# Kernel optimization log

Measured on AMD Instinct MI355X. Metric: run time of the kernel, lower is better.

The kernel has to match this reference:

```python
import jax, jax.numpy as jnp
import numpy as np
from jax.ops import segment_sum

N = 100000   # total nodes
M = 50000    # propagated subset size (len(index))
E = 600000   # edges over the subset graph
D = 128      # embedding_size
EPS = 1e-8
N_LAYERS = 3  # self.LayerNums


def setup_inputs() -> dict:
    key = jax.random.key(0)
    ks = jax.random.split(key, 12)
    features = jax.random.normal(ks[0], (N, D), dtype=jnp.float32)
    index = jnp.arange(M, dtype=jnp.int64)  # subset of nodes that get propagated
    edge_row = jax.random.randint(ks[1], (E,), 0, M, dtype=jnp.int64)
    edge_col = jax.random.randint(ks[2], (E,), 0, M, dtype=jnp.int64)
    edge_val = jax.random.uniform(ks[3], (E,), dtype=jnp.float32)
    # MLP prediction weights: D -> D//2 -> D//4 -> D//6 -> 1 (last no bias)
    def xavier(k, fan_in, fan_out):
        lim = jnp.sqrt(6.0 / (fan_in + fan_out)).astype(jnp.float32)
        return jax.random.uniform(k, (fan_in, fan_out), jnp.float32, -lim, lim)
    W1 = xavier(ks[4], D, D // 2); b1 = jnp.zeros((D // 2,), jnp.float32)
    W2 = xavier(ks[5], D // 2, D // 4); b2 = jnp.zeros((D // 4,), jnp.float32)
    W3 = xavier(ks[6], D // 4, D // 6); b3 = jnp.zeros((D // 6,), jnp.float32)
    W4 = xavier(ks[7], D // 6, 1)
    return {"features": features, "index": index, "edge_row": edge_row,
            "edge_col": edge_col, "edge_val": edge_val,
            "W1": W1, "b1": b1, "W2": W2, "b2": b2, "W3": W3, "b3": b3, "W4": W4}


def _gcn_layer(features, index, row, col, val):
    # symmetric normalization: d = rowsum(A)+eps; A' = d^-1/2 A d^-1/2
    deg = segment_sum(val, row, num_segments=M)
    d_inv_sqrt = jax.lax.rsqrt(deg + EPS)
    nval = val * d_inv_sqrt[row] * d_inv_sqrt[col]
    sub = features[index]                      # [M, D] subset_features
    msg = sub[col] * nval[:, None]             # [E, D]
    out = segment_sum(msg, row, num_segments=M)  # spmm -> [M, D]
    # new_features[index] = out; untouched rows keep original features
    return features.at[index].set(out)


def reference(features, index, edge_row, edge_col, edge_val,
              W1, b1, W2, b2, W3, b3, W4):
    x = features
    for _ in range(N_LAYERS):
        x = _gcn_layer(x, index, edge_row, edge_col, edge_val)
    # MLP prediction head (eval mode: dropout off), LeakyReLU slope 0.01
    h = jax.nn.leaky_relu(x @ W1 + b1, 0.01)
    h = jax.nn.leaky_relu(h @ W2 + b2, 0.01)
    h = jax.nn.leaky_relu(h @ W3 + b3, 0.01)
    return jax.nn.sigmoid(h @ W4)              # [N, 1]
```

## Files before the change

kernel.cpp:

```cpp
#include <hip/hip_runtime.h>
#include <math.h>

#define NN 100000
#define MM 50000
#define EE 600000
#define DD 128
#define NB 196

typedef short bf16x8 __attribute__((ext_vector_type(8)));
typedef float f32x4 __attribute__((ext_vector_type(4)));

__device__ __forceinline__ float bl(unsigned u) { return __uint_as_float(u << 16); }
__device__ __forceinline__ float bh(unsigned u) { return __uint_as_float(u & 0xFFFF0000u); }
__device__ __forceinline__ unsigned rne(float f) {
    unsigned u = __float_as_uint(f);
    return (u + 0x7FFFu + ((u >> 16) & 1u)) >> 16;
}
__device__ __forceinline__ unsigned pk2(float a, float b) { return rne(a) | (rne(b) << 16); }

__device__ __forceinline__ void fmab8(float v, uint4 u, float* a) {
    a[0] = fmaf(v, bl(u.x), a[0]); a[1] = fmaf(v, bh(u.x), a[1]);
    a[2] = fmaf(v, bl(u.y), a[2]); a[3] = fmaf(v, bh(u.y), a[3]);
    a[4] = fmaf(v, bl(u.z), a[4]); a[5] = fmaf(v, bh(u.z), a[5]);
    a[6] = fmaf(v, bl(u.w), a[6]); a[7] = fmaf(v, bh(u.w), a[7]);
}

__device__ __forceinline__ void fma21(float h, const float* wrow, float* a) {
    #pragma unroll
    for (int j = 0; j < 21; ++j) a[j] = fmaf(h, wrow[j], a[j]);
}

__global__ void deg_count_kernel(const int* __restrict__ row, const float* __restrict__ val,
                                 unsigned long long* __restrict__ dcpack,
                                 int* __restrict__ slot, int* __restrict__ invidx) {
    int e = blockIdx.x * 256 + threadIdx.x;
    if (e < NN) invidx[e] = -1;
    if (e < EE) {
        int r = row[e];
        unsigned long long add = (1ULL << 44) | (unsigned long long)(val[e] * 4294967296.0f);
        unsigned long long old = atomicAdd(&dcpack[r], add);
        slot[e] = (int)(old >> 44);
    }
}

__global__ void fused_setup_kernel(const unsigned long long* __restrict__ dcpack,
                                   float* __restrict__ dis,
                                   const int* __restrict__ index, int* __restrict__ invidx,
                                   int* __restrict__ cnt, int* __restrict__ partial,
                                   int* __restrict__ bsum) {
    __shared__ int ws[4];
    int tid = threadIdx.x, lane = tid & 63, w = tid >> 6;
    int i = blockIdx.x * 256 + tid;
    int v = 0;
    if (i < MM) {
        unsigned long long pkv = dcpack[i];
        v = (int)(pkv >> 44);
        float dsum = (float)(pkv & ((1ULL << 44) - 1)) * (1.0f / 4294967296.0f);
        dis[i] = rsqrtf(dsum + 1e-8f);
        invidx[index[i]] = i;
        cnt[i] = v;
    }
    int x = v;
    #pragma unroll
    for (int off = 1; off < 64; off <<= 1) {
        int t = __shfl_up(x, off, 64);
        if (lane >= off) x += t;
    }
    if (lane == 63) ws[w] = x;
    __syncthreads();
    int add = 0;
    for (int q = 0; q < w; ++q) add += ws[q];
    x += add;
    if (i < MM) partial[i] = x;
    if (tid == 255) bsum[blockIdx.x] = x;
}

__global__ void scanB_kernel(const int* __restrict__ bsum, int* __restrict__ boff) {
    int lane = threadIdx.x;
    int carry = 0;
    for (int base = 0; base < NB; base += 64) {
        int v = (base + lane < NB) ? bsum[base + lane] : 0;
        int x = v;
        #pragma unroll
        for (int off = 1; off < 64; off <<= 1) {
            int t = __shfl_up(x, off, 64);
            if (lane >= off) x += t;
        }
        if (base + lane < NB) boff[base + lane] = carry + x - v;
        carry += __shfl(x, 63);
    }
}

__global__ void scanC_kernel(const int* __restrict__ partial, const int* __restrict__ cnt,
                             const int* __restrict__ boff, int* __restrict__ rowptr) {
    int i = blockIdx.x * 256 + threadIdx.x;
    if (i < MM) rowptr[i] = partial[i] - cnt[i] + boff[i >> 8];
    if (i == 0) rowptr[MM] = EE;
}

__global__ void scatter_kernel(const int* __restrict__ row, const int* __restrict__ col,
                               const float* __restrict__ val, const float* __restrict__ dis,
                               const int* __restrict__ rowptr, const int* __restrict__ slot,
                               int* __restrict__ col_s, float* __restrict__ val_s) {
    int e = blockIdx.x * 256 + threadIdx.x;
    if (e < EE) {
        int r = row[e], c = col[e];
        int pos = rowptr[r] + slot[e];
        col_s[pos] = c;
        val_s[pos] = val[e] * dis[r] * dis[c];
    }
}

__global__ void cvt_kernel(const float* __restrict__ feat, const int* __restrict__ index,
                           unsigned* __restrict__ X0b,
                           const float* __restrict__ W1, const float* __restrict__ W2,
                           unsigned* __restrict__ W1b, unsigned* __restrict__ W2b) {
    int i = blockIdx.x * 256 + threadIdx.x;
    if (i < MM * 64) {
        int node = i >> 6, k2 = i & 63;
        int idx = index[node];
        float2 f = ((const float2*)feat)[(size_t)idx * 64 + k2];
        X0b[i] = pk2(f.x, f.y);
    }
    if (i < 4096) {
        int j = i >> 6, kp = i & 63;
        W1b[i] = pk2(W1[(2 * kp) * 64 + j], W1[(2 * kp + 1) * 64 + j]);
    } else if (i < 5120) {
        int u = i - 4096;
        int j = u >> 5, kp = u & 31;
        W2b[u] = pk2(W2[(2 * kp) * 32 + j], W2[(2 * kp + 1) * 32 + j]);
    }
}

__global__ __launch_bounds__(256) void spmm_kernel(
    const int* __restrict__ rowptr, const int* __restrict__ cols,
    const float* __restrict__ vals, const unsigned short* __restrict__ X,
    unsigned short* __restrict__ Y) {
    int lane = threadIdx.x & 63;
    int wid = threadIdx.x >> 6;
    int g = lane >> 4, sub = lane & 15;
    int r = blockIdx.x * 16 + wid * 4 + g;
    bool valid = (r < MM);
    int rc = valid ? r : (MM - 1);
    int s = rowptr[rc], e = rowptr[rc + 1];
    const uint4* __restrict__ X4 = (const uint4*)X;
    float a[8] = {0.f, 0.f, 0.f, 0.f, 0.f, 0.f, 0.f, 0.f};
    for (int base = s; base < e; base += 16) {
        int cnt = min(16, e - base);
        int c = 0; float v = 0.f;
        if (sub < cnt) { c = cols[base + sub]; v = vals[base + sub]; }
        int j = 0;
        for (; j + 4 <= cnt; j += 4) {
            int c0 = __shfl(c, g * 16 + j);     float v0 = __shfl(v, g * 16 + j);
            int c1 = __shfl(c, g * 16 + j + 1); float v1 = __shfl(v, g * 16 + j + 1);
            int c2 = __shfl(c, g * 16 + j + 2); float v2 = __shfl(v, g * 16 + j + 2);
            int c3 = __shfl(c, g * 16 + j + 3); float v3 = __shfl(v, g * 16 + j + 3);
            uint4 u0 = X4[(size_t)c0 * 16 + sub];
            uint4 u1 = X4[(size_t)c1 * 16 + sub];
            uint4 u2 = X4[(size_t)c2 * 16 + sub];
            uint4 u3 = X4[(size_t)c3 * 16 + sub];
            fmab8(v0, u0, a);
            fmab8(v1, u1, a);
            fmab8(v2, u2, a);
            fmab8(v3, u3, a);
        }
        for (; j < cnt; ++j) {
            int cc = __shfl(c, g * 16 + j); float vv = __shfl(v, g * 16 + j);
            uint4 u0 = X4[(size_t)cc * 16 + sub];
            fmab8(vv, u0, a);
        }
    }
    if (valid) {
        uint4 o;
        o.x = pk2(a[0], a[1]); o.y = pk2(a[2], a[3]);
        o.z = pk2(a[4], a[5]); o.w = pk2(a[6], a[7]);
        ((uint4*)Y)[(size_t)r * 16 + sub] = o;
    }
}

#define NPB 64
#define XDW 68
#define WDW 36

__global__ __launch_bounds__(256) void mlp_kernel(
    const float* __restrict__ feat, const unsigned short* __restrict__ X3,
    const int* __restrict__ invidx,
    const unsigned* __restrict__ W1b, const float* __restrict__ b1,
    const unsigned* __restrict__ W2b, const float* __restrict__ b2,
    const float* __restrict__ W3, const float* __restrict__ b3,
    const float* __restrict__ W4, float* __restrict__ out) {
    __shared__ unsigned smem[4352 + 4352 + 1152];
    unsigned* xs  = smem;
    float*    h1f = (float*)smem;
    unsigned* w1t = smem + 4352;
    float*    h2f = (float*)(smem + 4352);
    unsigned* w2t = smem + 4352 + 4352;

    int tid = threadIdx.x;
    int nb = blockIdx.x * NPB;

    #pragma unroll 4
    for (int it = 0; it < 16; ++it) {
        int i = it * 256 + tid;
        int node = i >> 6, u = i & 63;
        int n = nb + node;
        unsigned p = 0;
        if (n < NN) {
            int q = invidx[n];
            if (q >= 0) p = ((const unsigned*)X3)[(size_t)q * 64 + u];
            else { float2 f = ((const float2*)feat)[(size_t)n * 64 + u]; p = pk2(f.x, f.y); }
        }
        xs[node * XDW + u] = p;
    }
    #pragma unroll
    for (int it = 0; it < 4; ++it) {
        int i = it * 256 + tid;
        int j = i >> 4, s4 = i & 15;
        uint4 wv = ((const uint4*)W1b)[i];
        *(uint4*)(w1t + j * XDW + s4 * 4) = wv;
    }
    {
        int j = tid >> 3, s4 = tid & 7;
        uint4 wv = ((const uint4*)W2b)[tid];
        *(uint4*)(w2t + j * WDW + s4 * 4) = wv;
    }
    __syncthreads();

    int lane = tid & 63, w = tid >> 6;
    int p = lane & 15, q = lane >> 4;

    bf16x8 af[4];
    #pragma unroll
    for (int kc = 0; kc < 4; ++kc)
        af[kc] = *(const bf16x8*)((const short*)(xs + (w * 16 + p) * XDW + kc * 16 + q * 4));

    f32x4 acc[4];
    #pragma unroll
    for (int jt = 0; jt < 4; ++jt) {
        float bv = b1[jt * 16 + p];
        acc[jt][0] = bv; acc[jt][1] = bv; acc[jt][2] = bv; acc[jt][3] = bv;
    }
    #pragma unroll
    for (int jt = 0; jt < 4; ++jt) {
        #pragma unroll
        for (int kc = 0; kc < 4; ++kc) {
            bf16x8 bf = *(const bf16x8*)((const short*)(w1t + (jt * 16 + p) * XDW + kc * 16 + q * 4));
            acc[jt] = __builtin_amdgcn_mfma_f32_16x16x32_bf16(af[kc], bf, acc[jt], 0, 0, 0);
        }
    }
    __syncthreads();
    #pragma unroll
    for (int jt = 0; jt < 4; ++jt) {
        #pragma unroll
        for (int r = 0; r < 4; ++r) {
            float v = acc[jt][r];
            v = v > 0.f ? v : 0.01f * v;
            h1f[(w * 16 + q * 4 + r) * XDW + jt * 16 + p] = v;
        }
    }
    __syncthreads();

    bf16x8 a2f[2];
    #pragma unroll
    for (int kc = 0; kc < 2; ++kc) {
        const float* hp = h1f + (w * 16 + p) * XDW + kc * 32 + q * 8;
        f32x4 v0 = *(const f32x4*)hp;
        f32x4 v1 = *(const f32x4*)(hp + 4);
        unsigned u0 = pk2(v0[0], v0[1]), u1 = pk2(v0[2], v0[3]);
        unsigned u2 = pk2(v1[0], v1[1]), u3 = pk2(v1[2], v1[3]);
        uint4 uu = make_uint4(u0, u1, u2, u3);
        a2f[kc] = *(const bf16x8*)&uu;
    }
    f32x4 acc2[2];
    #pragma unroll
    for (int jt = 0; jt < 2; ++jt) {
        float bv = b2[jt * 16 + p];
        acc2[jt][0] = bv; acc2[jt][1] = bv; acc2[jt][2] = bv; acc2[jt][3] = bv;
        #pragma unroll
        for (int kc = 0; kc < 2; ++kc) {
            bf16x8 bf = *(const bf16x8*)((const short*)(w2t + (jt * 16 + p) * WDW + kc * 16 + q * 4));
            acc2[jt] = __builtin_amdgcn_mfma_f32_16x16x32_bf16(a2f[kc], bf, acc2[jt], 0, 0, 0);
        }
    }
    __syncthreads();
    #pragma unroll
    for (int jt = 0; jt < 2; ++jt) {
        #pragma unroll
        for (int r = 0; r < 4; ++r) {
            float v = acc2[jt][r];
            v = v > 0.f ? v : 0.01f * v;
            h2f[(w * 16 + q * 4 + r) * WDW + jt * 16 + p] = v;
        }
    }
    __syncthreads();

    int node = w * 16 + p;
    float a3[21];
    #pragma unroll
    for (int j = 0; j < 21; ++j) a3[j] = b3[j];
    #pragma unroll 4
    for (int k = 0; k < 32; ++k) {
        float hk = h2f[node * WDW + k];
        fma21(hk, W3 + k * 21, a3);
    }
    float s = 0.f;
    #pragma unroll
    for (int j = 0; j < 21; ++j) {
        float vj = a3[j] > 0.f ? a3[j] : 0.01f * a3[j];
        s = fmaf(vj, W4[j], s);
    }
    if (q == 0) {
        int n = nb + node;
        if (n < NN) out[n] = 1.f / (1.f + expf(-s));
    }
}

extern "C" void kernel_launch(void* const* d_in, const int* in_sizes, int n_in,
                              void* d_out, int out_size, void* d_ws, size_t ws_size,
                              hipStream_t stream) {
    const float* feat = (const float*)d_in[0];
    const int*   index = (const int*)d_in[1];
    const int*   erow = (const int*)d_in[2];
    const int*   ecol = (const int*)d_in[3];
    const float* evalp = (const float*)d_in[4];
    const float* W1 = (const float*)d_in[5];
    const float* b1 = (const float*)d_in[6];
    const float* W2 = (const float*)d_in[7];
    const float* b2 = (const float*)d_in[8];
    const float* W3 = (const float*)d_in[9];
    const float* b3 = (const float*)d_in[10];
    const float* W4 = (const float*)d_in[11];
    float* out = (float*)d_out;

    char* ws = (char*)d_ws;
    size_t off = 0;
    auto alloc = [&](size_t bytes) -> void* {
        void* p = ws + off;
        off += (bytes + 255) & ~(size_t)255;
        return p;
    };
    unsigned long long* dcpack = (unsigned long long*)alloc((size_t)MM * 8);
    float* dis     = (float*)alloc((size_t)MM * 4);
    int*   cnt     = (int*)  alloc((size_t)MM * 4);
    int*   rowptr  = (int*)  alloc((size_t)(MM + 1) * 4);
    int*   partial = (int*)  alloc((size_t)MM * 4);
    int*   bsum    = (int*)  alloc((size_t)NB * 4);
    int*   boff    = (int*)  alloc((size_t)NB * 4);
    int*   slot    = (int*)  alloc((size_t)EE * 4);
    int*   col_s   = (int*)  alloc((size_t)EE * 4);
    float* val_s   = (float*)alloc((size_t)EE * 4);
    int*   invidx  = (int*)  alloc((size_t)NN * 4);
    unsigned* W1b  = (unsigned*)alloc(4096 * 4);
    unsigned* W2b  = (unsigned*)alloc(1024 * 4);
    unsigned*       X0b = (unsigned*)      alloc((size_t)MM * DD * 2);
    unsigned short* Xa  = (unsigned short*)alloc((size_t)MM * DD * 2);
    unsigned short* Xb  = (unsigned short*)alloc((size_t)MM * DD * 2);

    hipMemsetAsync(dcpack, 0, (size_t)MM * 8, stream);

    deg_count_kernel<<<(EE + 255) / 256, 256, 0, stream>>>(erow, evalp, dcpack, slot, invidx);
    fused_setup_kernel<<<NB, 256, 0, stream>>>(dcpack, dis, index, invidx, cnt, partial, bsum);
    scanB_kernel<<<1, 64, 0, stream>>>(bsum, boff);
    scanC_kernel<<<(MM + 255) / 256, 256, 0, stream>>>(partial, cnt, boff, rowptr);
    scatter_kernel<<<(EE + 255) / 256, 256, 0, stream>>>(erow, ecol, evalp, dis,
                                                         rowptr, slot, col_s, val_s);
    cvt_kernel<<<(MM * 64 + 255) / 256, 256, 0, stream>>>(feat, index, X0b, W1, W2, W1b, W2b);

    spmm_kernel<<<(MM + 15) / 16, 256, 0, stream>>>(rowptr, col_s, val_s,
                                                    (const unsigned short*)X0b, Xa);
    spmm_kernel<<<(MM + 15) / 16, 256, 0, stream>>>(rowptr, col_s, val_s, Xa, Xb);
    spmm_kernel<<<(MM + 15) / 16, 256, 0, stream>>>(rowptr, col_s, val_s, Xb, Xa);

    mlp_kernel<<<(NN + NPB - 1) / NPB, 256, 0, stream>>>(feat, Xa, invidx,
                                                         W1b, b1, W2b, b2, W3, b3, W4, out);
}
```

Baseline: 269.9 us.

## Write final layer into full bf16 feature buffer and simplify MLP loads

The cvt kernel now also converts the untouched (non-indexed) feature rows to bf16 in a full-size buffer, and the last SpMM writes its rows through the index remap into that same buffer. The MLP kernel then reads a single contiguous bf16 matrix straight from global memory into MFMA operands, with no shared-memory staging of X and weights and no block-wide barriers, using per-wave scratch only. This removes the per-element invidx branch and the fp32 conversion from the MLP, at the cost of a larger cvt kernel over all N rows and an extra full-size workspace buffer.

After: 265.5 us. About the same (-1.6%).

```diff
diff --git a/kernel.cpp b/kernel.cpp
--- a/kernel.cpp
+++ b/kernel.cpp
@@ -6,6 +6,7 @@
 #define EE 600000
 #define DD 128
 #define NB 196
+#define NNP 100096
 
 typedef short bf16x8 __attribute__((ext_vector_type(8)));
 typedef float f32x4 __attribute__((ext_vector_type(4)));
@@ -112,30 +113,35 @@
 }
 
 __global__ void cvt_kernel(const float* __restrict__ feat, const int* __restrict__ index,
-                           unsigned* __restrict__ X0b,
+                           const int* __restrict__ invidx,
+                           unsigned* __restrict__ X0b, unsigned* __restrict__ Xfull,
                            const float* __restrict__ W1, const float* __restrict__ W2,
                            unsigned* __restrict__ W1b, unsigned* __restrict__ W2b) {
     int i = blockIdx.x * 256 + threadIdx.x;
+    int n = i >> 6, u = i & 63;
+    if (n < NN && invidx[n] < 0) {
+        float2 f = ((const float2*)feat)[(size_t)n * 64 + u];
+        Xfull[(size_t)n * 64 + u] = pk2(f.x, f.y);
+    }
     if (i < MM * 64) {
-        int node = i >> 6, k2 = i & 63;
-        int idx = index[node];
-        float2 f = ((const float2*)feat)[(size_t)idx * 64 + k2];
+        int idx = index[n];
+        float2 f = ((const float2*)feat)[(size_t)idx * 64 + u];
         X0b[i] = pk2(f.x, f.y);
     }
     if (i < 4096) {
         int j = i >> 6, kp = i & 63;
         W1b[i] = pk2(W1[(2 * kp) * 64 + j], W1[(2 * kp + 1) * 64 + j]);
     } else if (i < 5120) {
-        int u = i - 4096;
-        int j = u >> 5, kp = u & 31;
-        W2b[u] = pk2(W2[(2 * kp) * 32 + j], W2[(2 * kp + 1) * 32 + j]);
+        int t = i - 4096;
+        int j = t >> 5, kp = t & 31;
+        W2b[t] = pk2(W2[(2 * kp) * 32 + j], W2[(2 * kp + 1) * 32 + j]);
     }
 }
 
 __global__ __launch_bounds__(256) void spmm_kernel(
     const int* __restrict__ rowptr, const int* __restrict__ cols,
     const float* __restrict__ vals, const unsigned short* __restrict__ X,
-    unsigned short* __restrict__ Y) {
+    unsigned short* __restrict__ Y, const int* __restrict__ remap) {
     int lane = threadIdx.x & 63;
     int wid = threadIdx.x >> 6;
     int g = lane >> 4, sub = lane & 15;
@@ -171,69 +177,34 @@
         }
     }
     if (valid) {
+        int dst = remap ? remap[rc] : rc;
         uint4 o;
         o.x = pk2(a[0], a[1]); o.y = pk2(a[2], a[3]);
         o.z = pk2(a[4], a[5]); o.w = pk2(a[6], a[7]);
-        ((uint4*)Y)[(size_t)r * 16 + sub] = o;
-    }
-}
-
-#define NPB 64
-#define XDW 68
-#define WDW 36
+        ((uint4*)Y)[(size_t)dst * 16 + sub] = o;
+    }
+}
 
 __global__ __launch_bounds__(256) void mlp_kernel(
-    const float* __restrict__ feat, const unsigned short* __restrict__ X3,
-    const int* __restrict__ invidx,
+    const unsigned* __restrict__ Xfull,
     const unsigned* __restrict__ W1b, const float* __restrict__ b1,
     const unsigned* __restrict__ W2b, const float* __restrict__ b2,
     const float* __restrict__ W3, const float* __restrict__ b3,
     const float* __restrict__ W4, float* __restrict__ out) {
-    __shared__ unsigned smem[4352 + 4352 + 1152];
-    unsigned* xs  = smem;
-    float*    h1f = (float*)smem;
-    unsigned* w1t = smem + 4352;
-    float*    h2f = (float*)(smem + 4352);
-    unsigned* w2t = smem + 4352 + 4352;
-
+    __shared__ float hls[4 * 1088];
     int tid = threadIdx.x;
-    int nb = blockIdx.x * NPB;
-
-    #pragma unroll 4
-    for (int it = 0; it < 16; ++it) {
-        int i = it * 256 + tid;
-        int node = i >> 6, u = i & 63;
-        int n = nb + node;
-        unsigned p = 0;
-        if (n < NN) {
-            int q = invidx[n];
-            if (q >= 0) p = ((const unsigned*)X3)[(size_t)q * 64 + u];
-            else { float2 f = ((const float2*)feat)[(size_t)n * 64 + u]; p = pk2(f.x, f.y); }
-        }
-        xs[node * XDW + u] = p;
-    }
-    #pragma unroll
-    for (int it = 0; it < 4; ++it) {
-        int i = it * 256 + tid;
-        int j = i >> 4, s4 = i & 15;
-        uint4 wv = ((const uint4*)W1b)[i];
-        *(uint4*)(w1t + j * XDW + s4 * 4) = wv;
-    }
-    {
-        int j = tid >> 3, s4 = tid & 7;
-        uint4 wv = ((const uint4*)W2b)[tid];
-        *(uint4*)(w2t + j * WDW + s4 * 4) = wv;
-    }
-    __syncthreads();
-
     int lane = tid & 63, w = tid >> 6;
     int p = lane & 15, q = lane >> 4;
+    float* hw = hls + w * 1088;
+    int nb = blockIdx.x * 64;
+    int node = nb + w * 16 + p;
 
     bf16x8 af[4];
     #pragma unroll
-    for (int kc = 0; kc < 4; ++kc)
-        af[kc] = *(const bf16x8*)((const short*)(xs + (w * 16 + p) * XDW + kc * 16 + q * 4));
-
+    for (int kc = 0; kc < 4; ++kc) {
+        uint4 u = *(const uint4*)(Xfull + (size_t)node * 64 + kc * 16 + q * 4);
+        af[kc] = *(const bf16x8*)&u;
+    }
     f32x4 acc[4];
     #pragma unroll
     for (int jt = 0; jt < 4; ++jt) {
@@ -244,31 +215,28 @@
     for (int jt = 0; jt < 4; ++jt) {
         #pragma unroll
         for (int kc = 0; kc < 4; ++kc) {
-            bf16x8 bf = *(const bf16x8*)((const short*)(w1t + (jt * 16 + p) * XDW + kc * 16 + q * 4));
+            uint4 u = *(const uint4*)(W1b + (jt * 16 + p) * 64 + kc * 16 + q * 4);
+            bf16x8 bf = *(const bf16x8*)&u;
             acc[jt] = __builtin_amdgcn_mfma_f32_16x16x32_bf16(af[kc], bf, acc[jt], 0, 0, 0);
         }
     }
-    __syncthreads();
     #pragma unroll
     for (int jt = 0; jt < 4; ++jt) {
         #pragma unroll
         for (int r = 0; r < 4; ++r) {
             float v = acc[jt][r];
             v = v > 0.f ? v : 0.01f * v;
-            h1f[(w * 16 + q * 4 + r) * XDW + jt * 16 + p] = v;
-        }
-    }
-    __syncthreads();
-
+            hw[(q * 4 + r) * 68 + jt * 16 + p] = v;
+        }
+    }
     bf16x8 a2f[2];
     #pragma unroll
     for (int kc = 0; kc < 2; ++kc) {
-        const float* hp = h1f + (w * 16 + p) * XDW + kc * 32 + q * 8;
+        const float* hp = hw + p * 68 + kc * 32 + q * 8;
         f32x4 v0 = *(const f32x4*)hp;
         f32x4 v1 = *(const f32x4*)(hp + 4);
-        unsigned u0 = pk2(v0[0], v0[1]), u1 = pk2(v0[2], v0[3]);
-        unsigned u2 = pk2(v1[0], v1[1]), u3 = pk2(v1[2], v1[3]);
-        uint4 uu = make_uint4(u0, u1, u2, u3);
+        uint4 uu = make_uint4(pk2(v0[0], v0[1]), pk2(v0[2], v0[3]),
+                              pk2(v1[0], v1[1]), pk2(v1[2], v1[3]));
         a2f[kc] = *(const bf16x8*)&uu;
     }
     f32x4 acc2[2];
@@ -278,29 +246,26 @@
         acc2[jt][0] = bv; acc2[jt][1] = bv; acc2[jt][2] = bv; acc2[jt][3] = bv;
         #pragma unroll
         for (int kc = 0; kc < 2; ++kc) {
-            bf16x8 bf = *(const bf16x8*)((const short*)(w2t + (jt * 16 + p) * WDW + kc * 16 + q * 4));
+            uint4 u = *(const uint4*)(W2b + (jt * 16 + p) * 32 + kc * 16 + q * 4);
+            bf16x8 bf = *(const bf16x8*)&u;
             acc2[jt] = __builtin_amdgcn_mfma_f32_16x16x32_bf16(a2f[kc], bf, acc2[jt], 0, 0, 0);
         }
     }
-    __syncthreads();
     #pragma unroll
     for (int jt = 0; jt < 2; ++jt) {
         #pragma unroll
         for (int r = 0; r < 4; ++r) {
             float v = acc2[jt][r];
             v = v > 0.f ? v : 0.01f * v;
-            h2f[(w * 16 + q * 4 + r) * WDW + jt * 16 + p] = v;
-        }
-    }
-    __syncthreads();
-
-    int node = w * 16 + p;
+            hw[(q * 4 + r) * 36 + jt * 16 + p] = v;
+        }
+    }
     float a3[21];
     #pragma unroll
     for (int j = 0; j < 21; ++j) a3[j] = b3[j];
     #pragma unroll 4
     for (int k = 0; k < 32; ++k) {
-        float hk = h2f[node * WDW + k];
+        float hk = hw[p * 36 + k];
         fma21(hk, W3 + k * 21, a3);
     }
     float s = 0.f;
@@ -310,7 +275,7 @@
         s = fmaf(vj, W4[j], s);
     }
     if (q == 0) {
-        int n = nb + node;
+        int n = nb + w * 16 + p;
         if (n < NN) out[n] = 1.f / (1.f + expf(-s));
     }
 }
@@ -352,9 +317,10 @@
     int*   invidx  = (int*)  alloc((size_t)NN * 4);
     unsigned* W1b  = (unsigned*)alloc(4096 * 4);
     unsigned* W2b  = (unsigned*)alloc(1024 * 4);
-    unsigned*       X0b = (unsigned*)      alloc((size_t)MM * DD * 2);
-    unsigned short* Xa  = (unsigned short*)alloc((size_t)MM * DD * 2);
-    unsigned short* Xb  = (unsigned short*)alloc((size_t)MM * DD * 2);
+    unsigned*       X0b   = (unsigned*)      alloc((size_t)MM * DD * 2);
+    unsigned short* Xa    = (unsigned short*)alloc((size_t)MM * DD * 2);
+    unsigned short* Xb    = (unsigned short*)alloc((size_t)MM * DD * 2);
+    unsigned*       Xfull = (unsigned*)      alloc((size_t)NNP * DD * 2);
 
     hipMemsetAsync(dcpack, 0, (size_t)MM * 8, stream);
 
@@ -364,13 +330,15 @@
     scanC_kernel<<<(MM + 255) / 256, 256, 0, stream>>>(partial, cnt, boff, rowptr);
     scatter_kernel<<<(EE + 255) / 256, 256, 0, stream>>>(erow, ecol, evalp, dis,
                                                          rowptr, slot, col_s, val_s);
-    cvt_kernel<<<(MM * 64 + 255) / 256, 256, 0, stream>>>(feat, index, X0b, W1, W2, W1b, W2b);
+    cvt_kernel<<<(NN * 64 + 255) / 256, 256, 0, stream>>>(feat, index, invidx, X0b, Xfull,
+                                                          W1, W2, W1b, W2b);
 
     spmm_kernel<<<(MM + 15) / 16, 256, 0, stream>>>(rowptr, col_s, val_s,
-                                                    (const unsigned short*)X0b, Xa);
-    spmm_kernel<<<(MM + 15) / 16, 256, 0, stream>>>(rowptr, col_s, val_s, Xa, Xb);
-    spmm_kernel<<<(MM + 15) / 16, 256, 0, stream>>>(rowptr, col_s, val_s, Xb, Xa);
-
-    mlp_kernel<<<(NN + NPB - 1) / NPB, 256, 0, stream>>>(feat, Xa, invidx,
-                                                         W1b, b1, W2b, b2, W3, b3, W4, out);
-}
+                                                    (const unsigned short*)X0b, Xa, nullptr);
+    spmm_kernel<<<(MM + 15) / 16, 256, 0, stream>>>(rowptr, col_s, val_s, Xa, Xb, nullptr);
+    spmm_kernel<<<(MM + 15) / 16, 256, 0, stream>>>(rowptr, col_s, val_s, Xb,
+                                                    (unsigned short*)Xfull, index);
+
+    mlp_kernel<<<(NNP + 63) / 64, 256, 0, stream>>>(Xfull, W1b, b1, W2b, b2,
+                                                    W3, b3, W4, out);
+}
```
